# Optimization experiments

Hardware: AMD Instinct MI355X
Metric: run time of the kernel (lower is better)

Reference implementation:

```python
import jax, jax.numpy as jnp
import numpy as np

N = 100_000   # nodes
E = 3_200_000 # edges
F = 512       # input features
H = 64        # hidden
C = 64        # classes
K = 10        # APPNP propagation steps
ALPHA = 0.1


def setup_inputs() -> dict:
    key = jax.random.key(0)
    k0, k1, k2, k3 = jax.random.split(key, 4)
    x = jax.random.normal(k0, (N, F), dtype=jnp.float32)
    W1 = jax.random.normal(k1, (H, F), dtype=jnp.float32) / np.float32(np.sqrt(F))
    b1 = jnp.zeros((H,), dtype=jnp.float32)
    W2 = jax.random.normal(k2, (C, H), dtype=jnp.float32) / np.float32(np.sqrt(H))
    b2 = jnp.zeros((C,), dtype=jnp.float32)
    edge_index = jax.random.randint(k3, (2, E), 0, N, dtype=jnp.int64)
    return {"x": x, "W1": W1, "b1": b1, "W2": W2, "b2": b2, "edge_index": edge_index}


def reference(x, W1, b1, W2, b2, edge_index):
    src = edge_index[0]  # message source (x_j)
    dst = edge_index[1]  # aggregation target
    # GCN normalization with self-loops: deg_i = 1 + sum of incoming edge weights
    deg = jax.ops.segment_sum(jnp.ones((E,), x.dtype), dst, num_segments=N) + 1.0
    dinv = jax.lax.rsqrt(deg)
    norm = dinv[src] * dinv[dst]      # per-edge coefficient
    self_w = dinv * dinv              # self-loop coefficient d_i^{-1}

    # MLP (dropout is identity in eval mode)
    h = jax.nn.relu(x @ W1.T + b1)
    h = h @ W2.T + b2                 # [N, C]

    # APPNP: z <- (1-alpha) * A_hat z + alpha * h, repeated K times
    z = h
    for _ in range(K):
        agg = jax.ops.segment_sum(norm[:, None] * z[src], dst, num_segments=N)
        agg = agg + self_w[:, None] * z
        z = (1.0 - ALPHA) * agg + ALPHA * h

    return jax.nn.log_softmax(z, axis=1)
```

## Files before the change

### kernel.cpp

```cpp
#include <hip/hip_runtime.h>
#include <hip/hip_bf16.h>

#define N_NODES 100000
#define N_EDGES 3200000
#define F_IN    512
#define H_DIM   64
#define C_DIM   64
#define K_STEPS 10
#define ALPHA   0.1f
#define RSTRIDE 96
#define NBINS   256
#define BINW    391
#define SLOTS   16384
#define EPB     4096

typedef __attribute__((ext_vector_type(8))) short bf16x8;
typedef __attribute__((ext_vector_type(4))) float f32x4;

__device__ __forceinline__ float bf2f(ushort u) {
    union { unsigned int i; float f; } c; c.i = ((unsigned int)u) << 16; return c.f;
}
__device__ __forceinline__ ushort f2bf(float f) {
    union { float f; unsigned int i; } c; c.f = f;
    unsigned int lsb = (c.i >> 16) & 1u;
    unsigned int r = c.i + 0x7fffu + lsb;
    return (ushort)(r >> 16);
}
__device__ __forceinline__ uint cvtpk(float a, float b) {
    uint r;
    asm("v_cvt_pk_bf16_f32 %0, %1, %2" : "=v"(r) : "v"(a), "v"(b));
    return r;
}

__global__ __launch_bounds__(256) void binA_kernel(
    const int* __restrict__ src, const int* __restrict__ dst,
    int* __restrict__ gcursor, uint* __restrict__ staging, int e)
{
    __shared__ int cnt[NBINS], sbase[NBINS], loff[NBINS], gbase[NBINS];
    __shared__ int wsum[4];
    __shared__ uint recs[EPB];
    __shared__ uchar binarr[EPB];
    int t = threadIdx.x;
    cnt[t] = 0; loff[t] = 0;
    __syncthreads();

    int blk = blockIdx.x * EPB;
    int nhere = e - blk; nhere = (nhere < EPB) ? nhere : EPB;

    #pragma unroll
    for (int j = 0; j < EPB / 256; ++j) {
        int i = blk + j * 256 + t;
        if (i < e) atomicAdd(&cnt[dst[i] / BINW], 1);
    }
    __syncthreads();

    int lane = t & 63, w = t >> 6;
    int v = cnt[t], incl = v;
    #pragma unroll
    for (int off = 1; off < 64; off <<= 1) {
        int u = __shfl_up(incl, off);
        if (lane >= off) incl += u;
    }
    if (lane == 63) wsum[w] = incl;
    __syncthreads();
    int woff = 0;
    #pragma unroll
    for (int j = 0; j < 4; ++j) woff += (j < w) ? wsum[j] : 0;
    sbase[t] = woff + (incl - v);
    gbase[t] = (v > 0) ? atomicAdd(&gcursor[t], v) : 0;
    __syncthreads();

    #pragma unroll
    for (int j = 0; j < EPB / 256; ++j) {
        int i = blk + j * 256 + t;
        if (i < e) {
            int ss = src[i], dd = dst[i];
            int b = dd / BINW;
            int dl = dd - b * BINW;
            int idx = sbase[b] + atomicAdd(&loff[b], 1);
            recs[idx] = (uint)ss | ((uint)dl << 17);
            binarr[idx] = (uchar)b;
        }
    }
    __syncthreads();

    #pragma unroll
    for (int j = 0; j < EPB / 256; ++j) {
        int idx = j * 256 + t;
        if (idx < nhere) {
            int b = binarr[idx];
            int gp = gbase[b] + (idx - sbase[b]);
            if (gp < SLOTS)
                staging[(size_t)b * SLOTS + gp] = recs[idx];
        }
    }
}

__global__ __launch_bounds__(256) void binB_kernel(
    const int* __restrict__ gcursor, const uint* __restrict__ staging,
    int* __restrict__ deg, float* __restrict__ dinv, float* __restrict__ selfc,
    int* __restrict__ esrc, int n)
{
    __shared__ int dloc[BINW];
    int b = blockIdx.x, t = threadIdx.x;
    for (int i = t; i < BINW; i += 256) dloc[i] = 0;
    __syncthreads();

    int cnt = gcursor[b];
    cnt = (cnt < SLOTS) ? cnt : SLOTS;
    const uint* st = staging + (size_t)b * SLOTS;
    int nb = b * BINW;

    int j = t;
    for (; j + 768 < cnt; j += 1024) {
        uint p0 = st[j], p1 = st[j + 256], p2 = st[j + 512], p3 = st[j + 768];
        int d0 = p0 >> 17, d1 = p1 >> 17, d2 = p2 >> 17, d3 = p3 >> 17;
        int q0 = atomicAdd(&dloc[d0], 1);
        int q1 = atomicAdd(&dloc[d1], 1);
        int q2 = atomicAdd(&dloc[d2], 1);
        int q3 = atomicAdd(&dloc[d3], 1);
        if (q0 < RSTRIDE) esrc[(size_t)(nb + d0) * RSTRIDE + q0] = (int)(p0 & 0x1FFFFu);
        if (q1 < RSTRIDE) esrc[(size_t)(nb + d1) * RSTRIDE + q1] = (int)(p1 & 0x1FFFFu);
        if (q2 < RSTRIDE) esrc[(size_t)(nb + d2) * RSTRIDE + q2] = (int)(p2 & 0x1FFFFu);
        if (q3 < RSTRIDE) esrc[(size_t)(nb + d3) * RSTRIDE + q3] = (int)(p3 & 0x1FFFFu);
    }
    for (; j < cnt; j += 256) {
        uint p = st[j];
        int d = p >> 17;
        int q = atomicAdd(&dloc[d], 1);
        if (q < RSTRIDE) esrc[(size_t)(nb + d) * RSTRIDE + q] = (int)(p & 0x1FFFFu);
    }
    __syncthreads();
    for (int i = t; i < BINW; i += 256) {
        int node = nb + i;
        if (node < n) {
            int dg = dloc[i];
            deg[node] = dg;
            float d = rsqrtf((float)dg + 1.0f);
            dinv[node]  = d;
            selfc[node] = (1.0f - ALPHA) * d * d;
        }
    }
}

__global__ void cvt_w_kernel(const float* __restrict__ W1, const float* __restrict__ W2,
                             ushort* __restrict__ w1bf, ushort* __restrict__ w2bf) {
    int i = blockIdx.x * blockDim.x + threadIdx.x;
    if (i < 64 * 512) w1bf[i] = f2bf(W1[i]);
    if (i < 64 * 64)  w2bf[i] = f2bf(W2[i]);
}

__global__ __launch_bounds__(256, 3) void mlp_mfma_kernel(
    const float* __restrict__ x, const ushort* __restrict__ w1bf, const float* __restrict__ b1,
    const ushort* __restrict__ w2bf, const float* __restrict__ b2, const float* __restrict__ dinv,
    ushort* __restrict__ y0, ushort* __restrict__ g, int n)
{
    __shared__ ushort h1s[4 * 4096];
    __shared__ ushort w2s[64 * 64];
    __shared__ float  b1s[64], b2s[64];

    int t = threadIdx.x;
    #pragma unroll
    for (int i = 0; i < 2; ++i) {
        int chunk = i * 256 + t;
        int byte = chunk * 16;
        int row = byte >> 7;
        int dsti = byte ^ ((row & 7) << 4);
        *reinterpret_cast<uint4*>((char*)w2s + dsti) = reinterpret_cast<const uint4*>(w2bf)[chunk];
    }
    if (t < 64) { b1s[t] = b1[t]; b2s[t] = b2[t]; }
    __syncthreads();

    int wid = t >> 6;
    int l   = t & 63;
    int lr  = l & 15;
    int lk  = l >> 4;
    int rowbase = blockIdx.x * 256 + wid * 64;

    f32x4 acc[4][4] = {};
    for (int kk = 0; kk < 16; ++kk) {
        int k0 = kk * 32 + lk * 8;
        bf16x8 a[4];
        #pragma unroll
        for (int fr = 0; fr < 4; ++fr) {
            int row = rowbase + fr * 16 + lr;
            row = (row < n) ? row : (n - 1);
            const float* p = x + (size_t)row * F_IN + k0;
            f32x4 u0 = __builtin_nontemporal_load(reinterpret_cast<const f32x4*>(p));
            f32x4 u1 = __builtin_nontemporal_load(reinterpret_cast<const f32x4*>(p + 4));
            union { uint u[4]; bf16x8 v; } pk;
            pk.u[0] = cvtpk(u0[0], u0[1]);
            pk.u[1] = cvtpk(u0[2], u0[3]);
            pk.u[2] = cvtpk(u1[0], u1[1]);
            pk.u[3] = cvtpk(u1[2], u1[3]);
            a[fr] = pk.v;
        }
        bf16x8 b[4];
        #pragma unroll
        for (int fc = 0; fc < 4; ++fc) {
            int nn = fc * 16 + lr;
            b[fc] = *reinterpret_cast<const bf16x8*>(w1bf + (size_t)nn * F_IN + k0);
        }
        #pragma unroll
        for (int fr = 0; fr < 4; ++fr)
            #pragma unroll
            for (int fc = 0; fc < 4; ++fc)
                acc[fr][fc] = __builtin_amdgcn_mfma_f32_16x16x32_bf16(a[fr], b[fc], acc[fr][fc], 0, 0, 0);
    }

    ushort* h1w = h1s + wid * 4096;
    #pragma unroll
    for (int fr = 0; fr < 4; ++fr) {
        #pragma unroll
        for (int fc = 0; fc < 4; ++fc) {
            #pragma unroll
            for (int reg = 0; reg < 4; ++reg) {
                float vv = acc[fr][fc][reg] + b1s[fc * 16 + lr];
                vv = fmaxf(vv, 0.f);
                int row = fr * 16 + lk * 4 + reg;
                int col = fc * 16 + lr;
                int byte = row * 128 + col * 2;
                *reinterpret_cast<ushort*>((char*)h1w + (byte ^ ((row & 7) << 4))) = f2bf(vv);
            }
        }
    }

    f32x4 acc2[4][4] = {};
    #pragma unroll
    for (int kk = 0; kk < 2; ++kk) {
        int k0 = kk * 32 + lk * 8;
        bf16x8 a2[4], bb[4];
        #pragma unroll
        for (int fr = 0; fr < 4; ++fr) {
            int row = fr * 16 + lr;
            int byte = row * 128 + k0 * 2;
            a2[fr] = *reinterpret_cast<const bf16x8*>((char*)h1w + (byte ^ ((row & 7) << 4)));
        }
        #pragma unroll
        for (int fc = 0; fc < 4; ++fc) {
            int nn = fc * 16 + lr;
            int byte = nn * 128 + k0 * 2;
            bb[fc] = *reinterpret_cast<const bf16x8*>((char*)w2s + (byte ^ ((nn & 7) << 4)));
        }
        #pragma unroll
        for (int fr = 0; fr < 4; ++fr)
            #pragma unroll
            for (int fc = 0; fc < 4; ++fc)
                acc2[fr][fc] = __builtin_amdgcn_mfma_f32_16x16x32_bf16(a2[fr], bb[fc], acc2[fr][fc], 0, 0, 0);
    }

    #pragma unroll
    for (int fr = 0; fr < 4; ++fr) {
        #pragma unroll
        for (int fc = 0; fc < 4; ++fc) {
            #pragma unroll
            for (int reg = 0; reg < 4; ++reg) {
                int row = rowbase + fr * 16 + lk * 4 + reg;
                int col = fc * 16 + lr;
                if (row < n) {
                    float d = dinv[row];
                    float hv = (acc2[fr][fc][reg] + b2s[col]) * d;
                    size_t o = (size_t)row * 64 + col;
                    y0[o] = f2bf(hv);
                    g[o]  = f2bf(ALPHA * hv);
                }
            }
        }
    }
}

template<bool LAST>
__global__ __launch_bounds__(256) void appnp_step_kernel(
    const int* __restrict__ deg, const int* __restrict__ esrc,
    const float* __restrict__ selfc, const float* __restrict__ dinv,
    const ushort* __restrict__ yin, const ushort* __restrict__ g,
    ushort* __restrict__ yout, float* __restrict__ lsm, int n)
{
    int idx = blockIdx.x * blockDim.x + threadIdx.x;
    int wid = idx >> 6;
    if (wid >= n) return;
    int lane = threadIdx.x & 63;
    int q = lane >> 4;
    int p = lane & 15;
    const uint2* y2 = (const uint2*)yin;
    int cnt = deg[wid];
    cnt = (cnt < RSTRIDE) ? cnt : RSTRIDE;
    int base = wid * RSTRIDE;

    float a0 = 0.f, a1 = 0.f, a2 = 0.f, a3 = 0.f;
    int e = 0;
    for (; e + 15 < cnt; e += 16) {
        int s0 = __builtin_nontemporal_load(&esrc[base + e + q]);
        int s1 = __builtin_nontemporal_load(&esrc[base + e + 4 + q]);
        int s2 = __builtin_nontemporal_load(&esrc[base + e + 8 + q]);
        int s3 = __builtin_nontemporal_load(&esrc[base + e + 12 + q]);
        uint2 v0 = y2[(size_t)s0 * 16 + p];
        uint2 v1 = y2[(size_t)s1 * 16 + p];
        uint2 v2 = y2[(size_t)s2 * 16 + p];
        uint2 v3 = y2[(size_t)s3 * 16 + p];
        a0 += bf2f((ushort)v0.x) + bf2f((ushort)v1.x) + bf2f((ushort)v2.x) + bf2f((ushort)v3.x);
        a1 += bf2f((ushort)(v0.x >> 16)) + bf2f((ushort)(v1.x >> 16)) +
              bf2f((ushort)(v2.x >> 16)) + bf2f((ushort)(v3.x >> 16));
        a2 += bf2f((ushort)v0.y) + bf2f((ushort)v1.y) + bf2f((ushort)v2.y) + bf2f((ushort)v3.y);
        a3 += bf2f((ushort)(v0.y >> 16)) + bf2f((ushort)(v1.y >> 16)) +
              bf2f((ushort)(v2.y >> 16)) + bf2f((ushort)(v3.y >> 16));
    }
    for (; e < cnt; e += 4) {
        bool valid = (e + q) < cnt;
        int s = __builtin_nontemporal_load(&esrc[valid ? (base + e + q) : base]);
        uint2 v = y2[(size_t)s * 16 + p];
        a0 += valid ? bf2f((ushort)v.x) : 0.f;
        a1 += valid ? bf2f((ushort)(v.x >> 16)) : 0.f;
        a2 += valid ? bf2f((ushort)v.y) : 0.f;
        a3 += valid ? bf2f((ushort)(v.y >> 16)) : 0.f;
    }
    a0 += __shfl_xor(a0, 16); a0 += __shfl_xor(a0, 32);
    a1 += __shfl_xor(a1, 16); a1 += __shfl_xor(a1, 32);
    a2 += __shfl_xor(a2, 16); a2 += __shfl_xor(a2, 32);
    a3 += __shfl_xor(a3, 16); a3 += __shfl_xor(a3, 32);

    size_t o2 = (size_t)wid * 16 + p;
    uint2 ys = y2[o2];
    uint2 gg = ((const uint2*)g)[o2];
    float sc = selfc[wid];
    float yn0 = sc * (a0 + bf2f((ushort)ys.x)) + bf2f((ushort)gg.x);
    float yn1 = sc * (a1 + bf2f((ushort)(ys.x >> 16))) + bf2f((ushort)(gg.x >> 16));
    float yn2 = sc * (a2 + bf2f((ushort)ys.y)) + bf2f((ushort)gg.y);
    float yn3 = sc * (a3 + bf2f((ushort)(ys.y >> 16))) + bf2f((ushort)(gg.y >> 16));

    if (!LAST) {
        if (q == 0) {
            uint2 pk;
            pk.x = cvtpk(yn0, yn1);
            pk.y = cvtpk(yn2, yn3);
            ((uint2*)yout)[o2] = pk;
        }
    } else {
        float di = dinv[wid];
        float z0 = yn0 / di, z1 = yn1 / di, z2 = yn2 / di, z3 = yn3 / di;
        float m = fmaxf(fmaxf(z0, z1), fmaxf(z2, z3));
        #pragma unroll
        for (int off = 8; off > 0; off >>= 1) m = fmaxf(m, __shfl_xor(m, off));
        float s = expf(z0 - m) + expf(z1 - m) + expf(z2 - m) + expf(z3 - m);
        #pragma unroll
        for (int off = 8; off > 0; off >>= 1) s += __shfl_xor(s, off);
        float ls = logf(s);
        if (q == 0) {
            float4 wv = make_float4(z0 - m - ls, z1 - m - ls, z2 - m - ls, z3 - m - ls);
            *reinterpret_cast<float4*>(&lsm[(size_t)wid * 64 + 4 * p]) = wv;
        }
    }
}

extern "C" void kernel_launch(void* const* d_in, const int* in_sizes, int n_in,
                              void* d_out, int out_size, void* d_ws, size_t ws_size,
                              hipStream_t stream) {
    const float* x  = (const float*)d_in[0];
    const float* W1 = (const float*)d_in[1];
    const float* b1 = (const float*)d_in[2];
    const float* W2 = (const float*)d_in[3];
    const float* b2 = (const float*)d_in[4];
    const int*   ei = (const int*)d_in[5];
    const int* src = ei;
    const int* dst = ei + N_EDGES;
    float* out = (float*)d_out;

    char* ws = (char*)d_ws;
    size_t off = 0;
    auto alloc = [&](size_t bytes) -> void* {
        void* p = ws + off;
        off += (bytes + 255) & ~(size_t)255;
        return p;
    };
    int*    deg     = (int*)   alloc((size_t)N_NODES * 4);
    float*  dinv    = (float*) alloc((size_t)N_NODES * 4);
    float*  selfc   = (float*) alloc((size_t)N_NODES * 4);
    int*    gcursor = (int*)   alloc((size_t)NBINS * 4);
    uint*   staging = (uint*)  alloc((size_t)NBINS * SLOTS * 4);
    int*    esrc    = (int*)   alloc((size_t)N_NODES * RSTRIDE * 4);
    ushort* g       = (ushort*)alloc((size_t)N_NODES * 64 * 2);
    ushort* ya      = (ushort*)alloc((size_t)N_NODES * 64 * 2);
    ushort* yb      = (ushort*)alloc((size_t)N_NODES * 64 * 2);
    ushort* w1bf    = (ushort*)alloc((size_t)H_DIM * F_IN * 2);
    ushort* w2bf    = (ushort*)alloc((size_t)C_DIM * H_DIM * 2);

    hipMemsetAsync(gcursor, 0, (size_t)NBINS * 4, stream);
    binA_kernel<<<(N_EDGES + EPB - 1) / EPB, 256, 0, stream>>>(src, dst, gcursor, staging, N_EDGES);
    binB_kernel<<<NBINS, 256, 0, stream>>>(gcursor, staging, deg, dinv, selfc, esrc, N_NODES);
    cvt_w_kernel<<<(H_DIM * F_IN + 255) / 256, 256, 0, stream>>>(W1, W2, w1bf, w2bf);
    mlp_mfma_kernel<<<(N_NODES + 255) / 256, 256, 0, stream>>>(x, w1bf, b1, w2bf, b2, dinv,
                                                               ya, g, N_NODES);

    const int grid = (N_NODES * 64 + 255) / 256;
    ushort* yin = ya;
    ushort* yout = yb;
    for (int k = 0; k < K_STEPS - 1; ++k) {
        appnp_step_kernel<false><<<grid, 256, 0, stream>>>(
            deg, esrc, selfc, dinv, yin, g, yout, nullptr, N_NODES);
        ushort* tmp = yin; yin = yout; yout = tmp;
    }
    appnp_step_kernel<true><<<grid, 256, 0, stream>>>(
        deg, esrc, selfc, dinv, yin, g, nullptr, out, N_NODES);
}
```

Measured before the change: 904.2 us.

## Widen APPNP gathers to 16-byte rows and shrink MLP blocks to one wave

The propagation kernel now has each lane load a uint4 (8 bf16 features), so 8 lanes cover a 64-feature row and a wave processes 8 edges per gather instead of 4. This halves the number of load instructions per edge and widens each memory request, at the cost of more accumulator registers and one extra shuffle stage in the reduction. Separately, the MLP kernel switches to 64-thread blocks of one wavefront and reads W2 directly from global memory instead of staging it in shared memory. This gives a finer-grained grid and less shared memory per block.

```diff
diff --git a/kernel.cpp b/kernel.cpp
--- a/kernel.cpp
+++ b/kernel.cpp
@@ -150,32 +150,22 @@
     if (i < 64 * 64)  w2bf[i] = f2bf(W2[i]);
 }
 
-__global__ __launch_bounds__(256, 3) void mlp_mfma_kernel(
+__global__ __launch_bounds__(64, 4) void mlp_mfma_kernel(
     const float* __restrict__ x, const ushort* __restrict__ w1bf, const float* __restrict__ b1,
     const ushort* __restrict__ w2bf, const float* __restrict__ b2, const float* __restrict__ dinv,
     ushort* __restrict__ y0, ushort* __restrict__ g, int n)
 {
-    __shared__ ushort h1s[4 * 4096];
-    __shared__ ushort w2s[64 * 64];
+    __shared__ ushort h1s[4096];
     __shared__ float  b1s[64], b2s[64];
 
     int t = threadIdx.x;
-    #pragma unroll
-    for (int i = 0; i < 2; ++i) {
-        int chunk = i * 256 + t;
-        int byte = chunk * 16;
-        int row = byte >> 7;
-        int dsti = byte ^ ((row & 7) << 4);
-        *reinterpret_cast<uint4*>((char*)w2s + dsti) = reinterpret_cast<const uint4*>(w2bf)[chunk];
-    }
-    if (t < 64) { b1s[t] = b1[t]; b2s[t] = b2[t]; }
-    __syncthreads();
-
-    int wid = t >> 6;
-    int l   = t & 63;
-    int lr  = l & 15;
-    int lk  = l >> 4;
-    int rowbase = blockIdx.x * 256 + wid * 64;
+    b1s[t] = b1[t];
+    b2s[t] = b2[t];
+    __syncthreads();
+
+    int lr = t & 15;
+    int lk = t >> 4;
+    int rowbase = blockIdx.x * 64;
 
     f32x4 acc[4][4] = {};
     for (int kk = 0; kk < 16; ++kk) {
@@ -208,7 +198,6 @@
                 acc[fr][fc] = __builtin_amdgcn_mfma_f32_16x16x32_bf16(a[fr], b[fc], acc[fr][fc], 0, 0, 0);
     }
 
-    ushort* h1w = h1s + wid * 4096;
     #pragma unroll
     for (int fr = 0; fr < 4; ++fr) {
         #pragma unroll
@@ -220,10 +209,11 @@
                 int row = fr * 16 + lk * 4 + reg;
                 int col = fc * 16 + lr;
                 int byte = row * 128 + col * 2;
-                *reinterpret_cast<ushort*>((char*)h1w + (byte ^ ((row & 7) << 4))) = f2bf(vv);
+                *reinterpret_cast<ushort*>((char*)h1s + (byte ^ ((row & 7) << 4))) = f2bf(vv);
             }
         }
     }
+    __syncthreads();
 
     f32x4 acc2[4][4] = {};
     #pragma unroll
@@ -234,13 +224,12 @@
         for (int fr = 0; fr < 4; ++fr) {
             int row = fr * 16 + lr;
             int byte = row * 128 + k0 * 2;
-            a2[fr] = *reinterpret_cast<const bf16x8*>((char*)h1w + (byte ^ ((row & 7) << 4)));
+            a2[fr] = *reinterpret_cast<const bf16x8*>((char*)h1s + (byte ^ ((row & 7) << 4)));
         }
         #pragma unroll
         for (int fc = 0; fc < 4; ++fc) {
             int nn = fc * 16 + lr;
-            int byte = nn * 128 + k0 * 2;
-            bb[fc] = *reinterpret_cast<const bf16x8*>((char*)w2s + (byte ^ ((nn & 7) << 4)));
+            bb[fc] = *reinterpret_cast<const bf16x8*>(w2bf + (size_t)nn * H_DIM + k0);
         }
         #pragma unroll
         for (int fr = 0; fr < 4; ++fr)
@@ -280,74 +269,114 @@
     int wid = idx >> 6;
     if (wid >= n) return;
     int lane = threadIdx.x & 63;
-    int q = lane >> 4;
-    int p = lane & 15;
-    const uint2* y2 = (const uint2*)yin;
+    int q = lane >> 3;
+    int p = lane & 7;
+    const uint4* y4 = (const uint4*)yin;
     int cnt = deg[wid];
     cnt = (cnt < RSTRIDE) ? cnt : RSTRIDE;
     int base = wid * RSTRIDE;
 
     float a0 = 0.f, a1 = 0.f, a2 = 0.f, a3 = 0.f;
+    float a4 = 0.f, a5 = 0.f, a6 = 0.f, a7 = 0.f;
     int e = 0;
-    for (; e + 15 < cnt; e += 16) {
+    for (; e + 31 < cnt; e += 32) {
         int s0 = __builtin_nontemporal_load(&esrc[base + e + q]);
-        int s1 = __builtin_nontemporal_load(&esrc[base + e + 4 + q]);
-        int s2 = __builtin_nontemporal_load(&esrc[base + e + 8 + q]);
-        int s3 = __builtin_nontemporal_load(&esrc[base + e + 12 + q]);
-        uint2 v0 = y2[(size_t)s0 * 16 + p];
-        uint2 v1 = y2[(size_t)s1 * 16 + p];
-        uint2 v2 = y2[(size_t)s2 * 16 + p];
-        uint2 v3 = y2[(size_t)s3 * 16 + p];
+        int s1 = __builtin_nontemporal_load(&esrc[base + e + 8 + q]);
+        int s2 = __builtin_nontemporal_load(&esrc[base + e + 16 + q]);
+        int s3 = __builtin_nontemporal_load(&esrc[base + e + 24 + q]);
+        uint4 v0 = y4[(size_t)s0 * 8 + p];
+        uint4 v1 = y4[(size_t)s1 * 8 + p];
+        uint4 v2 = y4[(size_t)s2 * 8 + p];
+        uint4 v3 = y4[(size_t)s3 * 8 + p];
         a0 += bf2f((ushort)v0.x) + bf2f((ushort)v1.x) + bf2f((ushort)v2.x) + bf2f((ushort)v3.x);
         a1 += bf2f((ushort)(v0.x >> 16)) + bf2f((ushort)(v1.x >> 16)) +
               bf2f((ushort)(v2.x >> 16)) + bf2f((ushort)(v3.x >> 16));
         a2 += bf2f((ushort)v0.y) + bf2f((ushort)v1.y) + bf2f((ushort)v2.y) + bf2f((ushort)v3.y);
         a3 += bf2f((ushort)(v0.y >> 16)) + bf2f((ushort)(v1.y >> 16)) +
               bf2f((ushort)(v2.y >> 16)) + bf2f((ushort)(v3.y >> 16));
-    }
-    for (; e < cnt; e += 4) {
+        a4 += bf2f((ushort)v0.z) + bf2f((ushort)v1.z) + bf2f((ushort)v2.z) + bf2f((ushort)v3.z);
+        a5 += bf2f((ushort)(v0.z >> 16)) + bf2f((ushort)(v1.z >> 16)) +
+              bf2f((ushort)(v2.z >> 16)) + bf2f((ushort)(v3.z >> 16));
+        a6 += bf2f((ushort)v0.w) + bf2f((ushort)v1.w) + bf2f((ushort)v2.w) + bf2f((ushort)v3.w);
+        a7 += bf2f((ushort)(v0.w >> 16)) + bf2f((ushort)(v1.w >> 16)) +
+              bf2f((ushort)(v2.w >> 16)) + bf2f((ushort)(v3.w >> 16));
+    }
+    if (e + 15 < cnt) {
+        int s0 = __builtin_nontemporal_load(&esrc[base + e + q]);
+        int s1 = __builtin_nontemporal_load(&esrc[base + e + 8 + q]);
+        uint4 v0 = y4[(size_t)s0 * 8 + p];
+        uint4 v1 = y4[(size_t)s1 * 8 + p];
+        a0 += bf2f((ushort)v0.x) + bf2f((ushort)v1.x);
+        a1 += bf2f((ushort)(v0.x >> 16)) + bf2f((ushort)(v1.x >> 16));
+        a2 += bf2f((ushort)v0.y) + bf2f((ushort)v1.y);
+        a3 += bf2f((ushort)(v0.y >> 16)) + bf2f((ushort)(v1.y >> 16));
+        a4 += bf2f((ushort)v0.z) + bf2f((ushort)v1.z);
+        a5 += bf2f((ushort)(v0.z >> 16)) + bf2f((ushort)(v1.z >> 16));
+        a6 += bf2f((ushort)v0.w) + bf2f((ushort)v1.w);
+        a7 += bf2f((ushort)(v0.w >> 16)) + bf2f((ushort)(v1.w >> 16));
+        e += 16;
+    }
+    for (; e < cnt; e += 8) {
         bool valid = (e + q) < cnt;
         int s = __builtin_nontemporal_load(&esrc[valid ? (base + e + q) : base]);
-        uint2 v = y2[(size_t)s * 16 + p];
-        a0 += valid ? bf2f((ushort)v.x) : 0.f;
-        a1 += valid ? bf2f((ushort)(v.x >> 16)) : 0.f;
-        a2 += valid ? bf2f((ushort)v.y) : 0.f;
-        a3 += valid ? bf2f((ushort)(v.y >> 16)) : 0.f;
-    }
-    a0 += __shfl_xor(a0, 16); a0 += __shfl_xor(a0, 32);
-    a1 += __shfl_xor(a1, 16); a1 += __shfl_xor(a1, 32);
-    a2 += __shfl_xor(a2, 16); a2 += __shfl_xor(a2, 32);
-    a3 += __shfl_xor(a3, 16); a3 += __shfl_xor(a3, 32);
-
-    size_t o2 = (size_t)wid * 16 + p;
-    uint2 ys = y2[o2];
-    uint2 gg = ((const uint2*)g)[o2];
+        uint4 v = y4[(size_t)s * 8 + p];
+        if (valid) {
+            a0 += bf2f((ushort)v.x); a1 += bf2f((ushort)(v.x >> 16));
+            a2 += bf2f((ushort)v.y); a3 += bf2f((ushort)(v.y >> 16));
+            a4 += bf2f((ushort)v.z); a5 += bf2f((ushort)(v.z >> 16));
+            a6 += bf2f((ushort)v.w); a7 += bf2f((ushort)(v.w >> 16));
+        }
+    }
+    a0 += __shfl_xor(a0, 8); a0 += __shfl_xor(a0, 16); a0 += __shfl_xor(a0, 32);
+    a1 += __shfl_xor(a1, 8); a1 += __shfl_xor(a1, 16); a1 += __shfl_xor(a1, 32);
+    a2 += __shfl_xor(a2, 8); a2 += __shfl_xor(a2, 16); a2 += __shfl_xor(a2, 32);
+    a3 += __shfl_xor(a3, 8); a3 += __shfl_xor(a3, 16); a3 += __shfl_xor(a3, 32);
+    a4 += __shfl_xor(a4, 8); a4 += __shfl_xor(a4, 16); a4 += __shfl_xor(a4, 32);
+    a5 += __shfl_xor(a5, 8); a5 += __shfl_xor(a5, 16); a5 += __shfl_xor(a5, 32);
+    a6 += __shfl_xor(a6, 8); a6 += __shfl_xor(a6, 16); a6 += __shfl_xor(a6, 32);
+    a7 += __shfl_xor(a7, 8); a7 += __shfl_xor(a7, 16); a7 += __shfl_xor(a7, 32);
+
+    size_t o4 = (size_t)wid * 8 + p;
+    uint4 ys = y4[o4];
+    uint4 gg = ((const uint4*)g)[o4];
     float sc = selfc[wid];
     float yn0 = sc * (a0 + bf2f((ushort)ys.x)) + bf2f((ushort)gg.x);
     float yn1 = sc * (a1 + bf2f((ushort)(ys.x >> 16))) + bf2f((ushort)(gg.x >> 16));
     float yn2 = sc * (a2 + bf2f((ushort)ys.y)) + bf2f((ushort)gg.y);
     float yn3 = sc * (a3 + bf2f((ushort)(ys.y >> 16))) + bf2f((ushort)(gg.y >> 16));
+    float yn4 = sc * (a4 + bf2f((ushort)ys.z)) + bf2f((ushort)gg.z);
+    float yn5 = sc * (a5 + bf2f((ushort)(ys.z >> 16))) + bf2f((ushort)(gg.z >> 16));
+    float yn6 = sc * (a6 + bf2f((ushort)ys.w)) + bf2f((ushort)gg.w);
+    float yn7 = sc * (a7 + bf2f((ushort)(ys.w >> 16))) + bf2f((ushort)(gg.w >> 16));
 
     if (!LAST) {
         if (q == 0) {
-            uint2 pk;
+            uint4 pk;
             pk.x = cvtpk(yn0, yn1);
             pk.y = cvtpk(yn2, yn3);
-            ((uint2*)yout)[o2] = pk;
+            pk.z = cvtpk(yn4, yn5);
+            pk.w = cvtpk(yn6, yn7);
+            ((uint4*)yout)[o4] = pk;
         }
     } else {
         float di = dinv[wid];
         float z0 = yn0 / di, z1 = yn1 / di, z2 = yn2 / di, z3 = yn3 / di;
-        float m = fmaxf(fmaxf(z0, z1), fmaxf(z2, z3));
-        #pragma unroll
-        for (int off = 8; off > 0; off >>= 1) m = fmaxf(m, __shfl_xor(m, off));
-        float s = expf(z0 - m) + expf(z1 - m) + expf(z2 - m) + expf(z3 - m);
-        #pragma unroll
-        for (int off = 8; off > 0; off >>= 1) s += __shfl_xor(s, off);
+        float z4 = yn4 / di, z5 = yn5 / di, z6 = yn6 / di, z7 = yn7 / di;
+        float m = fmaxf(fmaxf(fmaxf(z0, z1), fmaxf(z2, z3)),
+                        fmaxf(fmaxf(z4, z5), fmaxf(z6, z7)));
+        #pragma unroll
+        for (int off = 4; off > 0; off >>= 1) m = fmaxf(m, __shfl_xor(m, off));
+        float s = expf(z0 - m) + expf(z1 - m) + expf(z2 - m) + expf(z3 - m) +
+                  expf(z4 - m) + expf(z5 - m) + expf(z6 - m) + expf(z7 - m);
+        #pragma unroll
+        for (int off = 4; off > 0; off >>= 1) s += __shfl_xor(s, off);
         float ls = logf(s);
         if (q == 0) {
-            float4 wv = make_float4(z0 - m - ls, z1 - m - ls, z2 - m - ls, z3 - m - ls);
-            *reinterpret_cast<float4*>(&lsm[(size_t)wid * 64 + 4 * p]) = wv;
+            float* o = &lsm[(size_t)wid * 64 + 8 * p];
+            *reinterpret_cast<float4*>(o)     = make_float4(z0 - m - ls, z1 - m - ls,
+                                                            z2 - m - ls, z3 - m - ls);
+            *reinterpret_cast<float4*>(o + 4) = make_float4(z4 - m - ls, z5 - m - ls,
+                                                            z6 - m - ls, z7 - m - ls);
         }
     }
 }
@@ -388,8 +417,8 @@
     binA_kernel<<<(N_EDGES + EPB - 1) / EPB, 256, 0, stream>>>(src, dst, gcursor, staging, N_EDGES);
     binB_kernel<<<NBINS, 256, 0, stream>>>(gcursor, staging, deg, dinv, selfc, esrc, N_NODES);
     cvt_w_kernel<<<(H_DIM * F_IN + 255) / 256, 256, 0, stream>>>(W1, W2, w1bf, w2bf);
-    mlp_mfma_kernel<<<(N_NODES + 255) / 256, 256, 0, stream>>>(x, w1bf, b1, w2bf, b2, dinv,
-                                                               ya, g, N_NODES);
+    mlp_mfma_kernel<<<(N_NODES + 63) / 64, 64, 0, stream>>>(x, w1bf, b1, w2bf, b2, dinv,
+                                                            ya, g, N_NODES);
 
     const int grid = (N_NODES * 64 + 255) / 256;
     ushort* yin = ya;
```

Result: faster. 752.0 us (-16.8%).
